# Kernel optimization log

Measured on AMD Instinct MI355X. Metric: run time of the kernel, lower is better.

The kernel has to match this reference:

```python
import jax, jax.numpy as jnp
import numpy as np


def _conv2d(x, w, b, pad, rhs_dilation=(1, 1)):
    out = jax.lax.conv_general_dilated(
        x, w, window_strides=(1, 1),
        padding=((pad, pad), (pad, pad)),
        rhs_dilation=rhs_dilation,
        dimension_numbers=('NCHW', 'OIHW', 'NCHW'))
    return out + b[None, :, None, None]


def _bilinear(img, gx, gy):
    # img [C,H,W]; gx,gy [9,h,w] in [-1,1]; grid_sample bilinear, align_corners=True.
    # Coords are pre-clamped to [-1,1] so all samples are in-bounds; clamped
    # neighbor indices get zero bilinear weight at the boundary, matching torch.
    C, H, W = img.shape
    ix = (gx + 1.0) * 0.5 * (W - 1)
    iy = (gy + 1.0) * 0.5 * (H - 1)
    x0 = jnp.floor(ix)
    y0 = jnp.floor(iy)
    wx = ix - x0
    wy = iy - y0
    x0i = jnp.clip(x0.astype(jnp.int32), 0, W - 1)
    x1i = jnp.clip(x0i + 1, 0, W - 1)
    y0i = jnp.clip(y0.astype(jnp.int32), 0, H - 1)
    y1i = jnp.clip(y0i + 1, 0, H - 1)
    v00 = img[:, y0i, x0i]
    v01 = img[:, y0i, x1i]
    v10 = img[:, y1i, x0i]
    v11 = img[:, y1i, x1i]
    return (v00 * (1 - wx) * (1 - wy) + v01 * wx * (1 - wy)
            + v10 * (1 - wx) * wy + v11 * wx * wy)  # [C,9,h,w]


def _forward(x, conv_w, conv_b, offset_w, offset_b, mod_w, mod_b):
    b, c, h, w = x.shape
    offset = _conv2d(x, offset_w, offset_b, pad=1)          # [b,18,h,w]
    gx = jnp.clip(offset[:, :9] + jnp.linspace(-1.0, 1.0, w)[None, None, None, :], -1.0, 1.0)
    gy = jnp.clip(offset[:, 9:] + jnp.linspace(-1.0, 1.0, h)[None, None, :, None], -1.0, 1.0)
    sampled = jax.vmap(_bilinear)(x, gx, gy)                # [b,c,9,h,w]
    mod = _conv2d(x, mod_w, mod_b, pad=1)                   # [b,9,h,w]
    interp = sampled * mod[:, None]                         # [b,c,9,h,w]
    # tile the 9 samples into a 3h x 3w spatial grid: sample k = i + j*3 goes to block (j, i)
    tiled = interp.reshape(b, c, 3, 3, h, w).transpose(0, 1, 2, 4, 3, 5).reshape(b, c, 3 * h, 3 * w)
    # dilated 3x3 conv with dilation (h+1, w+1), stride 1, padding 1 -> [b,oc,h,w]
    return _conv2d(tiled, conv_w, conv_b, pad=1, rhs_dilation=(h + 1, w + 1))


def setup_inputs() -> dict:
    key = jax.random.key(0)
    ks = jax.random.split(key, 7)
    B, C, OC, H, W = 8, 256, 256, 64, 64
    return {
        'x': jax.random.normal(ks[0], (B, C, H, W), jnp.float32),
        'conv_w': jax.random.normal(ks[1], (OC, C, 3, 3), jnp.float32) * 0.02,
        'conv_b': jax.random.normal(ks[2], (OC,), jnp.float32) * 0.02,
        'offset_w': jax.random.normal(ks[3], (18, C, 3, 3), jnp.float32) * 0.01,
        'offset_b': jax.random.normal(ks[4], (18,), jnp.float32) * 0.01,
        'mod_w': jax.random.normal(ks[5], (9, C, 3, 3), jnp.float32) * 0.02,
        'mod_b': jax.random.normal(ks[6], (9,), jnp.float32) * 0.02,
    }


def reference(x, conv_w, conv_b, offset_w, offset_b, mod_w, mod_b):
    return _forward(x, conv_w, conv_b, offset_w, offset_b, mod_w, mod_b)
```

## Files before the change

kernel.cpp:

```cpp
#include <hip/hip_runtime.h>

typedef __attribute__((ext_vector_type(8))) _Float16 f16x8;
typedef __attribute__((ext_vector_type(4))) float f32x4;

#define CB 8
#define CC 256
#define CHW 4096


__global__ __launch_bounds__(256) void prep_k(const float* __restrict__ convw,
                                              const float* __restrict__ offw,
                                              const float* __restrict__ modw,
                                              _Float16* __restrict__ wAf,
                                              _Float16* __restrict__ wAomF) {
    int i = blockIdx.x * 256 + threadIdx.x;
    {
        int lane = i & 63, tile = (i >> 6) & 15, cc = (i >> 10) & 7, t = i >> 13;
        int oc = tile * 16 + (lane & 15);
        int cb = cc * 32 + (lane >> 4) * 8;
        f16x8 v;
#pragma unroll
        for (int j = 0; j < 8; ++j)
            v[j] = (_Float16)convw[oc * 2304 + (cb + j) * 9 + t];
        *(f16x8*)(wAf + (size_t)i * 8) = v;
    }
    if (i < 9216) {
        int lane = i & 63, tile = (i >> 6) & 1, cc = (i >> 7) & 7, t = i >> 10;
        int mr = tile * 16 + (lane & 15);
        int cb = cc * 32 + (lane >> 4) * 8;
        f16x8 u;
#pragma unroll
        for (int j = 0; j < 8; ++j) {
            int c = cb + j;
            float vv = 0.f;
            if (mr < 18) vv = offw[(mr * 256 + c) * 9 + t];
            else if (mr < 27) vv = modw[((mr - 18) * 256 + c) * 9 + t];
            u[j] = (_Float16)vv;
        }
        *(f16x8*)(wAomF + (size_t)i * 8) = u;
    }
}

__global__ __launch_bounds__(256) void xk(const float* __restrict__ x,
                                          _Float16* __restrict__ xt) {
    __shared__ ushort tile[64][264];
    int bid = blockIdx.x;
    int b = bid & 7, pos0 = (bid >> 3) << 6;
    int tid = threadIdx.x;
    int p = tid & 63;
    const float* xb = x + ((size_t)b << 20);
#pragma unroll 4
    for (int rep = 0; rep < 64; rep++) {
        int c = rep * 4 + (tid >> 6);
        _Float16 h = (_Float16)xb[((size_t)c << 12) + pos0 + p];
        tile[p][c] = __builtin_bit_cast(ushort, h);
    }
    __syncthreads();
    _Float16* xtb = xt + ((size_t)b << 20);
#pragma unroll
    for (int rep = 0; rep < 8; rep++) {
        int item = rep * 256 + tid;
        int pp = item >> 5, ch = item & 31;
        f16x8 v = *(const f16x8*)((const char*)&tile[0][0] + pp * 528 + ch * 16);
        *(f16x8*)((char*)xtb + (((size_t)(pos0 + pp)) << 9) + ch * 16) = v;
    }
}

__global__ __launch_bounds__(256) void k1(const _Float16* __restrict__ xt,
                                          const _Float16* __restrict__ wAomF,
                                          const float* __restrict__ offb,
                                          const float* __restrict__ modb,
                                          float4* __restrict__ descW,
                                          int4* __restrict__ descO) {
    __shared__ float sEp[32][68];

    int bid = blockIdx.x;
    int b = bid & 7, y = bid >> 3;
    int tid = threadIdx.x;
    int lane = tid & 63;
    int w = __builtin_amdgcn_readfirstlane(tid >> 6);
    int l15 = lane & 15, oct = lane >> 4;

    const _Float16* xtb = xt + ((size_t)b << 20);
    int kylo = (y == 0) ? 1 : 0;
    int kyhi = (y == 63) ? 1 : 2;

    f32x4 acc[2];
    acc[0] = (f32x4)0.f;
    acc[1] = (f32x4)0.f;
    f16x8 Z = {};

    int px = (w << 4) + l15;

    for (int ty = kylo; ty <= kyhi; ++ty) {
        int yy = y + ty - 1;
#pragma unroll
        for (int tx = 0; tx < 3; ++tx) {
            int t = ty * 3 + tx;
            int xx = px + tx - 1;
            bool val = (xx >= 0 && xx < 64);
            int xxc = min(max(xx, 0), 63);
            const f16x8* bp = (const f16x8*)(xtb + (((yy << 6) + xxc) << 8) + oct * 8);
            const f16x8* wf = (const f16x8*)wAomF + (size_t)t * 16 * 64 + lane;
#pragma unroll
            for (int c0 = 0; c0 < 256; c0 += 32) {
                f16x8 bf = bp[c0 >> 3];
                if (!val) bf = Z;
                int cc = c0 >> 5;
#pragma unroll
                for (int m = 0; m < 2; m++) {
                    f16x8 af = wf[(cc * 2 + m) * 64];
                    acc[m] = __builtin_amdgcn_mfma_f32_16x16x32_f16(af, bf, acc[m], 0, 0, 0);
                }
            }
        }
    }

#pragma unroll
    for (int m = 0; m < 2; m++) {
#pragma unroll
        for (int r = 0; r < 4; r++) {
            int row = (m << 4) + (oct << 2) + r;
            if (row < 27) sEp[row][px] = acc[m][r];
        }
    }
    __syncthreads();

    int g = tid >> 6;
    int xx2 = tid & 63;
    if (g < 3) {
        float lx = -1.0f + xx2 * (2.0f / 63.0f);
        float ly = -1.0f + y * (2.0f / 63.0f);
#pragma unroll
        for (int j = 0; j < 3; j++) {
            int k = g * 3 + j;
            float gx = sEp[k][xx2] + offb[k] + lx;
            gx = fminf(fmaxf(gx, -1.f), 1.f);
            float gy = sEp[9 + k][xx2] + offb[9 + k] + ly;
            gy = fminf(fmaxf(gy, -1.f), 1.f);
            float m = sEp[18 + k][xx2] + modb[k];
            float ix = (gx + 1.0f) * 0.5f * 63.0f;
            float iy = (gy + 1.0f) * 0.5f * 63.0f;
            float fx = floorf(ix), fy = floorf(iy);
            float wx = ix - fx, wy = iy - fy;
            int x0 = min(max((int)fx, 0), 63);
            int x1 = min(x0 + 1, 63);
            int y0 = min(max((int)fy, 0), 63);
            int y1 = min(y0 + 1, 63);
            float w00 = (1.f - wx) * (1.f - wy) * m;
            float w01 = wx * (1.f - wy) * m;
            float w10 = (1.f - wx) * wy * m;
            float w11 = wx * wy * m;
            int di = ((b * 9 + k) << 12) + (y << 6) + xx2;
            descW[di] = make_float4(w00, w01, w10, w11);
            descO[di] = make_int4(((y0 << 6) + x0) << 9, ((y0 << 6) + x1) << 9,
                                  ((y1 << 6) + x0) << 9, ((y1 << 6) + x1) << 9);
        }
    }
}

struct SmK2 {
    char cmb[2][2][8192];
    float4 dW[2][64];
    int4 dO[2][64];
};
__global__ __launch_bounds__(512, 4) void k2(const _Float16* __restrict__ xt,
                                             const _Float16* __restrict__ wAf,
                                             const float4* __restrict__ descW,
                                             const int4* __restrict__ descO,
                                             const float* __restrict__ convb,
                                             float* __restrict__ out) {
    __shared__ union SU {
        SmK2 m;
        f32x4 sred[2048];
    } S;

    int bid = blockIdx.x;
    int b = bid & 7, oy = bid >> 3;
    int tid = threadIdx.x;
    int l = tid & 63;
    int wid = __builtin_amdgcn_readfirstlane(tid >> 6);
    int mgrp = wid & 3, ks = wid >> 2;
    int oct = l >> 4, l15 = l & 15;

    const char* xtb = (const char*)(xt + ((size_t)b << 20));

    f32x4 acc[4][4];
#pragma unroll
    for (int mt = 0; mt < 4; mt++)
#pragma unroll
        for (int nt = 0; nt < 4; nt++) acc[mt][nt] = (f32x4)0.f;

    int p_ox = (tid >> 3) & 63;
    int p_cs = tid & 7;
    int csl = (p_ox << 7) + ((p_cs ^ (p_ox & 7)) << 4);
    const char* xtb_cs = xtb + p_cs * 16;

    int boff = (l15 << 7) + ((((ks << 2) + oct) ^ (l15 & 7)) << 4);

    auto stage_desc = [&](int t) {
        int slot = t & 1;
        int xx = tid;
        int ky = t / 3, kx = t % 3;
        int yy = oy + ky - 1;
        int xp = xx + kx - 1;
        float4 w4s = make_float4(0.f, 0.f, 0.f, 0.f);
        int4 o4 = make_int4(0, 0, 0, 0);
        if (yy >= 0 && yy < 64 && xp >= 0 && xp < 64) {
            int di = ((b * 9 + t) << 12) + (yy << 6) + xp;
            w4s = descW[di];
            o4 = descO[di];
        }
        S.m.dW[slot][xx] = w4s;
        S.m.dO[slot][xx] = o4;
    };

    int rdo0, rdo1, rdo2, rdo3;
    _Float16 rh0, rh1, rh2, rh3;
    auto refresh_desc = [&](int t) {
        int slot = t & 1;
        int4 o4 = S.m.dO[slot][p_ox];
        rdo0 = o4.x; rdo1 = o4.y; rdo2 = o4.z; rdo3 = o4.w;
        float4 w4 = S.m.dW[slot][p_ox];
        rh0 = (_Float16)w4.x; rh1 = (_Float16)w4.y;
        rh2 = (_Float16)w4.z; rh3 = (_Float16)w4.w;
    };

    auto issue_q = [&](f16x8* cr, int q) {
        const char* base = xtb_cs + (q << 7);
        cr[0] = *(const f16x8*)(base + rdo0);
        cr[1] = *(const f16x8*)(base + rdo1);
        cr[2] = *(const f16x8*)(base + rdo2);
        cr[3] = *(const f16x8*)(base + rdo3);
    };

    auto comb_write = [&](const f16x8* cr, char* dst) {
        f16x8 W0 = {rh0, rh0, rh0, rh0, rh0, rh0, rh0, rh0};
        f16x8 W1 = {rh1, rh1, rh1, rh1, rh1, rh1, rh1, rh1};
        f16x8 W2 = {rh2, rh2, rh2, rh2, rh2, rh2, rh2, rh2};
        f16x8 W3 = {rh3, rh3, rh3, rh3, rh3, rh3, rh3, rh3};
        f16x8 r = cr[0] * W0 + cr[1] * W1 + cr[2] * W2 + cr[3] * W3;
        *(f16x8*)(dst + csl) = r;
    };

    auto load_afr = [&](f16x8* afr, int m) {
        int t = m >> 2, q = m & 3;
        const f16x8* wf = (const f16x8*)wAf +
                          ((size_t)((t * 8 + q * 2 + ks) * 16 + mgrp * 4)) * 64 + l;
        afr[0] = wf[0];
        afr[1] = wf[64];
        afr[2] = wf[128];
        afr[3] = wf[192];
    };

    auto do_mfma = [&](const char* src, const f16x8* afr) {
        f16x8 bfr[4];
#pragma unroll
        for (int nt = 0; nt < 4; ++nt)
            bfr[nt] = *(const f16x8*)(src + boff + (nt << 11));
#pragma unroll
        for (int nt = 0; nt < 4; ++nt)
#pragma unroll
            for (int mt = 0; mt < 4; ++mt)
                acc[mt][nt] = __builtin_amdgcn_mfma_f32_16x16x32_f16(
                    afr[mt], bfr[nt], acc[mt][nt], 0, 0, 0);
    };

    if (tid < 64) stage_desc(0);
    __syncthreads();
    refresh_desc(0);
    {
        f16x8 c0[4];
        issue_q(c0, 0);
        comb_write(c0, S.m.cmb[0][0]);
        issue_q(c0, 1);
        comb_write(c0, S.m.cmb[0][1]);
    }
    __syncthreads();

    for (int P = 0; P < 18; ++P) {
        int pb = P & 1;
        int t = P >> 1;
        bool more = (P < 17);

        if (!(P & 1)) {
            if (t + 1 <= 8 && tid < 64) stage_desc(t + 1);
        } else if (more) {
            refresh_desc((P + 1) >> 1);
        }

        f16x8 afr[4];
        f16x8 cr[4];

        load_afr(afr, 2 * P);
        if (more) issue_q(cr, (2 * P + 2) & 3);
        do_mfma(S.m.cmb[pb][0], afr);
        load_afr(afr, 2 * P + 1);
        if (more) comb_write(cr, S.m.cmb[pb ^ 1][0]);

        if (more) issue_q(cr, (2 * P + 3) & 3);
        do_mfma(S.m.cmb[pb][1], afr);
        if (more) comb_write(cr, S.m.cmb[pb ^ 1][1]);

        __syncthreads();
    }

#pragma unroll
    for (int R = 0; R < 2; ++R) {
        if (ks == 1) {
#pragma unroll
            for (int mtl = 0; mtl < 2; ++mtl) {
#pragma unroll
                for (int nt = 0; nt < 4; ++nt) {
                    int fi = (((mgrp << 1) + mtl) << 8) + (((nt << 4) + l15) << 2) + oct;
                    S.sred[fi] = acc[(R << 1) + mtl][nt];
                }
            }
        }
        __syncthreads();
        if (ks == 0) {
#pragma unroll
            for (int mtl = 0; mtl < 2; ++mtl) {
#pragma unroll
                for (int nt = 0; nt < 4; ++nt) {
                    int fi = (((mgrp << 1) + mtl) << 8) + (((nt << 4) + l15) << 2) + oct;
                    acc[(R << 1) + mtl][nt] += S.sred[fi];
                }
            }
        }
        __syncthreads();
    }

    if (ks == 0) {
        size_t outb = ((size_t)b << 20);
#pragma unroll
        for (int mt = 0; mt < 4; ++mt) {
#pragma unroll
            for (int nt = 0; nt < 4; ++nt) {
                int ox = (nt << 4) + l15;
#pragma unroll
                for (int r = 0; r < 4; ++r) {
                    int oc = (mgrp << 6) + (mt << 4) + (oct << 2) + r;
                    out[outb + (size_t)oc * 4096 + (oy << 6) + ox] = acc[mt][nt][r] + convb[oc];
                }
            }
        }
    }
}

extern "C" void kernel_launch(void* const* d_in, const int* in_sizes, int n_in,
                              void* d_out, int out_size, void* d_ws, size_t ws_size,
                              hipStream_t stream) {
    const float* x     = (const float*)d_in[0];
    const float* convw = (const float*)d_in[1];
    const float* convb = (const float*)d_in[2];
    const float* offw  = (const float*)d_in[3];
    const float* offb  = (const float*)d_in[4];
    const float* modw  = (const float*)d_in[5];
    const float* modb  = (const float*)d_in[6];
    float* out = (float*)d_out;

    char* ws = (char*)d_ws;
    _Float16* wAf   = (_Float16*)(ws);
    _Float16* wAomF = (_Float16*)(ws + 1179648);
    float4*   descW = (float4*)(ws + 1327104);
    int4*     descO = (int4*)(ws + 6045696);
    _Float16* xt    = (_Float16*)(ws + 10764288);

    hipLaunchKernelGGL(prep_k, dim3(288), dim3(256), 0, stream, convw, offw, modw, wAf, wAomF);
    hipLaunchKernelGGL(xk, dim3(512), dim3(256), 0, stream, x, xt);
    hipLaunchKernelGGL(k1, dim3(512), dim3(256), 0, stream, xt, wAomF, offb, modb, descW, descO);
    hipLaunchKernelGGL(k2, dim3(512), dim3(512), 0, stream, xt, wAf, descW, descO, convb, out);
}
```

Baseline: 103.1 us.

## Deepen k2 software pipeline with register-prefetched descriptors and double-buffered A fragments

Restructures the main loop of k2 so that gathers for the next half-stage are issued a full iteration ahead. A-fragment weights are double-buffered in registers (afrA/afrB), and descriptor global loads are split from their shared-memory stores so their latency is hidden across the MFMA work. Each phase now processes two 8KB combine chunks at once. This raises register pressure, so launch bounds drop from 4 to 2 blocks per CU, trading occupancy for more instruction-level overlap.

```diff
diff --git a/kernel.cpp b/kernel.cpp
--- a/kernel.cpp
+++ b/kernel.cpp
@@ -160,11 +160,11 @@
 }
 
 struct SmK2 {
-    char cmb[2][2][8192];
+    char cmb[2][16384];
     float4 dW[2][64];
     int4 dO[2][64];
 };
-__global__ __launch_bounds__(512, 4) void k2(const _Float16* __restrict__ xt,
+__global__ __launch_bounds__(512, 2) void k2(const _Float16* __restrict__ xt,
                                              const _Float16* __restrict__ wAf,
                                              const float4* __restrict__ descW,
                                              const int4* __restrict__ descO,
@@ -198,25 +198,29 @@
 
     int boff = (l15 << 7) + ((((ks << 2) + oct) ^ (l15 & 7)) << 4);
 
-    auto stage_desc = [&](int t) {
-        int slot = t & 1;
-        int xx = tid;
+    float4 sdw;
+    int4 sdo;
+    auto stage_load = [&](int t) {
         int ky = t / 3, kx = t % 3;
         int yy = oy + ky - 1;
-        int xp = xx + kx - 1;
-        float4 w4s = make_float4(0.f, 0.f, 0.f, 0.f);
-        int4 o4 = make_int4(0, 0, 0, 0);
+        int xp = tid + kx - 1;
+        sdw = make_float4(0.f, 0.f, 0.f, 0.f);
+        sdo = make_int4(0, 0, 0, 0);
         if (yy >= 0 && yy < 64 && xp >= 0 && xp < 64) {
             int di = ((b * 9 + t) << 12) + (yy << 6) + xp;
-            w4s = descW[di];
-            o4 = descO[di];
-        }
-        S.m.dW[slot][xx] = w4s;
-        S.m.dO[slot][xx] = o4;
+            sdw = descW[di];
+            sdo = descO[di];
+        }
+    };
+    auto stage_store = [&](int t) {
+        int slot = t & 1;
+        S.m.dW[slot][tid] = sdw;
+        S.m.dO[slot][tid] = sdo;
     };
 
     int rdo0, rdo1, rdo2, rdo3;
     _Float16 rh0, rh1, rh2, rh3;
+    _Float16 rc0, rc1, rc2, rc3;
     auto refresh_desc = [&](int t) {
         int slot = t & 1;
         int4 o4 = S.m.dO[slot][p_ox];
@@ -226,83 +230,102 @@
         rh2 = (_Float16)w4.z; rh3 = (_Float16)w4.w;
     };
 
-    auto issue_q = [&](f16x8* cr, int q) {
-        const char* base = xtb_cs + (q << 7);
-        cr[0] = *(const f16x8*)(base + rdo0);
-        cr[1] = *(const f16x8*)(base + rdo1);
-        cr[2] = *(const f16x8*)(base + rdo2);
-        cr[3] = *(const f16x8*)(base + rdo3);
-    };
-
-    auto comb_write = [&](const f16x8* cr, char* dst) {
-        f16x8 W0 = {rh0, rh0, rh0, rh0, rh0, rh0, rh0, rh0};
-        f16x8 W1 = {rh1, rh1, rh1, rh1, rh1, rh1, rh1, rh1};
-        f16x8 W2 = {rh2, rh2, rh2, rh2, rh2, rh2, rh2, rh2};
-        f16x8 W3 = {rh3, rh3, rh3, rh3, rh3, rh3, rh3, rh3};
-        f16x8 r = cr[0] * W0 + cr[1] * W1 + cr[2] * W2 + cr[3] * W3;
-        *(f16x8*)(dst + csl) = r;
-    };
-
-    auto load_afr = [&](f16x8* afr, int m) {
-        int t = m >> 2, q = m & 3;
-        const f16x8* wf = (const f16x8*)wAf +
-                          ((size_t)((t * 8 + q * 2 + ks) * 16 + mgrp * 4)) * 64 + l;
-        afr[0] = wf[0];
-        afr[1] = wf[64];
-        afr[2] = wf[128];
-        afr[3] = wf[192];
-    };
-
-    auto do_mfma = [&](const char* src, const f16x8* afr) {
-        f16x8 bfr[4];
-#pragma unroll
-        for (int nt = 0; nt < 4; ++nt)
-            bfr[nt] = *(const f16x8*)(src + boff + (nt << 11));
-#pragma unroll
-        for (int nt = 0; nt < 4; ++nt)
-#pragma unroll
-            for (int mt = 0; mt < 4; ++mt)
-                acc[mt][nt] = __builtin_amdgcn_mfma_f32_16x16x32_f16(
-                    afr[mt], bfr[nt], acc[mt][nt], 0, 0, 0);
-    };
-
-    if (tid < 64) stage_desc(0);
+    f16x8 cr[4][2];
+    auto issue_G = [&](int h) {
+        const char* base = xtb_cs + (h << 8);
+#pragma unroll
+        for (int j = 0; j < 2; ++j) {
+            cr[0][j] = *(const f16x8*)(base + rdo0 + j * 128);
+            cr[1][j] = *(const f16x8*)(base + rdo1 + j * 128);
+            cr[2][j] = *(const f16x8*)(base + rdo2 + j * 128);
+            cr[3][j] = *(const f16x8*)(base + rdo3 + j * 128);
+        }
+        rc0 = rh0; rc1 = rh1; rc2 = rh2; rc3 = rh3;
+    };
+
+    auto combine = [&](char* dst) {
+        f16x8 W0 = {rc0, rc0, rc0, rc0, rc0, rc0, rc0, rc0};
+        f16x8 W1 = {rc1, rc1, rc1, rc1, rc1, rc1, rc1, rc1};
+        f16x8 W2 = {rc2, rc2, rc2, rc2, rc2, rc2, rc2, rc2};
+        f16x8 W3 = {rc3, rc3, rc3, rc3, rc3, rc3, rc3, rc3};
+#pragma unroll
+        for (int j = 0; j < 2; ++j) {
+            f16x8 r = cr[0][j] * W0 + cr[1][j] * W1 + cr[2][j] * W2 + cr[3][j] * W3;
+            *(f16x8*)(dst + (j << 13) + csl) = r;
+        }
+    };
+
+    auto load_afr = [&](f16x8 (&afr)[2][4], int Pn) {
+        int t = Pn >> 1, h = Pn & 1;
+#pragma unroll
+        for (int j = 0; j < 2; ++j) {
+            int q = 2 * h + j;
+            const f16x8* wf = (const f16x8*)wAf +
+                              ((size_t)((t * 8 + q * 2 + ks) * 16 + mgrp * 4)) * 64 + l;
+            afr[j][0] = wf[0];
+            afr[j][1] = wf[64];
+            afr[j][2] = wf[128];
+            afr[j][3] = wf[192];
+        }
+    };
+
+    auto do_mfma = [&](const char* src, f16x8 (&afr)[2][4]) {
+#pragma unroll
+        for (int j = 0; j < 2; ++j) {
+            f16x8 bfr[4];
+#pragma unroll
+            for (int nt = 0; nt < 4; ++nt)
+                bfr[nt] = *(const f16x8*)(src + (j << 13) + boff + (nt << 11));
+#pragma unroll
+            for (int nt = 0; nt < 4; ++nt)
+#pragma unroll
+                for (int mt = 0; mt < 4; ++mt)
+                    acc[mt][nt] = __builtin_amdgcn_mfma_f32_16x16x32_f16(
+                        afr[j][mt], bfr[nt], acc[mt][nt], 0, 0, 0);
+        }
+    };
+
+    f16x8 afrA[2][4], afrB[2][4];
+
+    if (tid < 64) {
+        stage_load(0);
+        stage_store(0);
+        stage_load(1);
+        stage_store(1);
+    }
     __syncthreads();
     refresh_desc(0);
-    {
-        f16x8 c0[4];
-        issue_q(c0, 0);
-        comb_write(c0, S.m.cmb[0][0]);
-        issue_q(c0, 1);
-        comb_write(c0, S.m.cmb[0][1]);
-    }
+    issue_G(0);
+    load_afr(afrA, 0);
+    combine(S.m.cmb[0]);
+    issue_G(1);
     __syncthreads();
 
-    for (int P = 0; P < 18; ++P) {
+    auto body = [&](int P, f16x8 (&cur)[2][4], f16x8 (&nxt)[2][4]) {
         int pb = P & 1;
-        int t = P >> 1;
-        bool more = (P < 17);
-
-        if (!(P & 1)) {
-            if (t + 1 <= 8 && tid < 64) stage_desc(t + 1);
-        } else if (more) {
-            refresh_desc((P + 1) >> 1);
-        }
-
-        f16x8 afr[4];
-        f16x8 cr[4];
-
-        load_afr(afr, 2 * P);
-        if (more) issue_q(cr, (2 * P + 2) & 3);
-        do_mfma(S.m.cmb[pb][0], afr);
-        load_afr(afr, 2 * P + 1);
-        if (more) comb_write(cr, S.m.cmb[pb ^ 1][0]);
-
-        if (more) issue_q(cr, (2 * P + 3) & 3);
-        do_mfma(S.m.cmb[pb][1], afr);
-        if (more) comb_write(cr, S.m.cmb[pb ^ 1][1]);
+        bool odd = (P & 1) != 0;
+
+        if (odd && P <= 13 && tid < 64) stage_load((P + 3) >> 1);
+
+        if (P < 17) combine(S.m.cmb[pb ^ 1]);
+
+        if (P < 16 && !odd) refresh_desc((P >> 1) + 1);
+
+        if (P < 16) issue_G(pb);
+
+        if (P < 17) load_afr(nxt, P + 1);
+
+        do_mfma(S.m.cmb[pb], cur);
+
+        if (odd && P <= 13 && tid < 64) stage_store((P + 3) >> 1);
 
         __syncthreads();
+    };
+
+#pragma unroll 1
+    for (int PP = 0; PP < 9; ++PP) {
+        body(2 * PP, afrA, afrB);
+        body(2 * PP + 1, afrB, afrA);
     }
 
 #pragma unroll
```

Measured after the change: 108.2 us. 1.05x slower.

## Merge weight-prep and transpose kernels, split work into finer blocks

Applied to the files above, without the earlier changes.

Merges the weight-conversion kernel and the x-transpose kernel into one launch, so one kernel launch and one inter-kernel gap go away. The transpose now handles half the channels per block, which doubles its block count and shrinks its shared tile. k1 is split into half-row blocks of 128 threads, giving twice as many blocks with smaller LDS. The main k2 loop also gets unroll 2, which risks raising register pressure.

```diff
diff --git a/kernel.cpp b/kernel.cpp
--- a/kernel.cpp
+++ b/kernel.cpp
@@ -8,74 +8,81 @@
 #define CHW 4096
 
 
-__global__ __launch_bounds__(256) void prep_k(const float* __restrict__ convw,
-                                              const float* __restrict__ offw,
-                                              const float* __restrict__ modw,
-                                              _Float16* __restrict__ wAf,
-                                              _Float16* __restrict__ wAomF) {
-    int i = blockIdx.x * 256 + threadIdx.x;
-    {
-        int lane = i & 63, tile = (i >> 6) & 15, cc = (i >> 10) & 7, t = i >> 13;
-        int oc = tile * 16 + (lane & 15);
-        int cb = cc * 32 + (lane >> 4) * 8;
-        f16x8 v;
-#pragma unroll
-        for (int j = 0; j < 8; ++j)
-            v[j] = (_Float16)convw[oc * 2304 + (cb + j) * 9 + t];
-        *(f16x8*)(wAf + (size_t)i * 8) = v;
-    }
-    if (i < 9216) {
-        int lane = i & 63, tile = (i >> 6) & 1, cc = (i >> 7) & 7, t = i >> 10;
-        int mr = tile * 16 + (lane & 15);
-        int cb = cc * 32 + (lane >> 4) * 8;
-        f16x8 u;
-#pragma unroll
-        for (int j = 0; j < 8; ++j) {
-            int c = cb + j;
-            float vv = 0.f;
-            if (mr < 18) vv = offw[(mr * 256 + c) * 9 + t];
-            else if (mr < 27) vv = modw[((mr - 18) * 256 + c) * 9 + t];
-            u[j] = (_Float16)vv;
-        }
-        *(f16x8*)(wAomF + (size_t)i * 8) = u;
-    }
-}
-
-__global__ __launch_bounds__(256) void xk(const float* __restrict__ x,
-                                          _Float16* __restrict__ xt) {
-    __shared__ ushort tile[64][264];
+__global__ __launch_bounds__(256) void pxk(const float* __restrict__ x,
+                                           const float* __restrict__ convw,
+                                           const float* __restrict__ offw,
+                                           const float* __restrict__ modw,
+                                           _Float16* __restrict__ wAf,
+                                           _Float16* __restrict__ wAomF,
+                                           _Float16* __restrict__ xt) {
+    __shared__ ushort tile[64][136];
     int bid = blockIdx.x;
-    int b = bid & 7, pos0 = (bid >> 3) << 6;
     int tid = threadIdx.x;
+
+    if (bid < 288) {
+        int i = bid * 256 + tid;
+        {
+            int lane = i & 63, tl = (i >> 6) & 15, cc = (i >> 10) & 7, t = i >> 13;
+            int oc = tl * 16 + (lane & 15);
+            int cb = cc * 32 + (lane >> 4) * 8;
+            f16x8 v;
+#pragma unroll
+            for (int j = 0; j < 8; ++j)
+                v[j] = (_Float16)convw[oc * 2304 + (cb + j) * 9 + t];
+            *(f16x8*)(wAf + (size_t)i * 8) = v;
+        }
+        if (i < 9216) {
+            int lane = i & 63, tl = (i >> 6) & 1, cc = (i >> 7) & 7, t = i >> 10;
+            int mr = tl * 16 + (lane & 15);
+            int cb = cc * 32 + (lane >> 4) * 8;
+            f16x8 u;
+#pragma unroll
+            for (int j = 0; j < 8; ++j) {
+                int c = cb + j;
+                float vv = 0.f;
+                if (mr < 18) vv = offw[(mr * 256 + c) * 9 + t];
+                else if (mr < 27) vv = modw[((mr - 18) * 256 + c) * 9 + t];
+                u[j] = (_Float16)vv;
+            }
+            *(f16x8*)(wAomF + (size_t)i * 8) = u;
+        }
+        return;
+    }
+
+    int nb = bid - 288;
+    int b = nb & 7, g = nb >> 3;
+    int pos0 = (g >> 1) << 6;
+    int ch0 = (g & 1) << 7;
     int p = tid & 63;
     const float* xb = x + ((size_t)b << 20);
 #pragma unroll 4
-    for (int rep = 0; rep < 64; rep++) {
-        int c = rep * 4 + (tid >> 6);
+    for (int rep = 0; rep < 32; rep++) {
+        int c = ch0 + rep * 4 + (tid >> 6);
         _Float16 h = (_Float16)xb[((size_t)c << 12) + pos0 + p];
-        tile[p][c] = __builtin_bit_cast(ushort, h);
+        tile[p][c - ch0] = __builtin_bit_cast(ushort, h);
     }
     __syncthreads();
     _Float16* xtb = xt + ((size_t)b << 20);
 #pragma unroll
-    for (int rep = 0; rep < 8; rep++) {
+    for (int rep = 0; rep < 4; rep++) {
         int item = rep * 256 + tid;
-        int pp = item >> 5, ch = item & 31;
-        f16x8 v = *(const f16x8*)((const char*)&tile[0][0] + pp * 528 + ch * 16);
-        *(f16x8*)((char*)xtb + (((size_t)(pos0 + pp)) << 9) + ch * 16) = v;
+        int pp = item >> 4, c16 = item & 15;
+        f16x8 v = *(const f16x8*)((const char*)&tile[0][0] + pp * 272 + c16 * 16);
+        *(f16x8*)((char*)xtb + (((size_t)(pos0 + pp)) << 9) + (ch0 << 1) + (c16 << 4)) = v;
     }
 }
 
-__global__ __launch_bounds__(256) void k1(const _Float16* __restrict__ xt,
+__global__ __launch_bounds__(128) void k1(const _Float16* __restrict__ xt,
                                           const _Float16* __restrict__ wAomF,
                                           const float* __restrict__ offb,
                                           const float* __restrict__ modb,
                                           float4* __restrict__ descW,
                                           int4* __restrict__ descO) {
-    __shared__ float sEp[32][68];
+    __shared__ float sEp[32][36];
 
     int bid = blockIdx.x;
-    int b = bid & 7, y = bid >> 3;
+    int b = bid & 7, yx = bid >> 3;
+    int y = yx >> 1, xh = yx & 1;
     int tid = threadIdx.x;
     int lane = tid & 63;
     int w = __builtin_amdgcn_readfirstlane(tid >> 6);
@@ -90,7 +97,8 @@
     acc[1] = (f32x4)0.f;
     f16x8 Z = {};
 
-    int px = (w << 4) + l15;
+    int pxl = (w << 4) + l15;
+    int px = (xh << 5) + pxl;
 
     for (int ty = kylo; ty <= kyhi; ++ty) {
         int yy = y + ty - 1;
@@ -121,24 +129,25 @@
 #pragma unroll
         for (int r = 0; r < 4; r++) {
             int row = (m << 4) + (oct << 2) + r;
-            if (row < 27) sEp[row][px] = acc[m][r];
+            if (row < 27) sEp[row][pxl] = acc[m][r];
         }
     }
     __syncthreads();
 
-    int g = tid >> 6;
-    int xx2 = tid & 63;
-    if (g < 3) {
+    int gq = tid >> 5;
+    int xl = tid & 31;
+    if (gq < 3) {
+        int xx2 = (xh << 5) + xl;
         float lx = -1.0f + xx2 * (2.0f / 63.0f);
         float ly = -1.0f + y * (2.0f / 63.0f);
 #pragma unroll
         for (int j = 0; j < 3; j++) {
-            int k = g * 3 + j;
-            float gx = sEp[k][xx2] + offb[k] + lx;
+            int k = gq * 3 + j;
+            float gx = sEp[k][xl] + offb[k] + lx;
             gx = fminf(fmaxf(gx, -1.f), 1.f);
-            float gy = sEp[9 + k][xx2] + offb[9 + k] + ly;
+            float gy = sEp[9 + k][xl] + offb[9 + k] + ly;
             gy = fminf(fmaxf(gy, -1.f), 1.f);
-            float m = sEp[18 + k][xx2] + modb[k];
+            float m = sEp[18 + k][xl] + modb[k];
             float ix = (gx + 1.0f) * 0.5f * 63.0f;
             float iy = (gy + 1.0f) * 0.5f * 63.0f;
             float fx = floorf(ix), fy = floorf(iy);
@@ -278,6 +287,7 @@
     }
     __syncthreads();
 
+#pragma unroll 2
     for (int P = 0; P < 18; ++P) {
         int pb = P & 1;
         int t = P >> 1;
@@ -367,8 +377,7 @@
     int4*     descO = (int4*)(ws + 6045696);
     _Float16* xt    = (_Float16*)(ws + 10764288);
 
-    hipLaunchKernelGGL(prep_k, dim3(288), dim3(256), 0, stream, convw, offw, modw, wAf, wAomF);
-    hipLaunchKernelGGL(xk, dim3(512), dim3(256), 0, stream, x, xt);
-    hipLaunchKernelGGL(k1, dim3(512), dim3(256), 0, stream, xt, wAomF, offb, modb, descW, descO);
+    hipLaunchKernelGGL(pxk, dim3(1312), dim3(256), 0, stream, x, convw, offw, modw, wAf, wAomF, xt);
+    hipLaunchKernelGGL(k1, dim3(1024), dim3(128), 0, stream, xt, wAomF, offb, modb, descW, descO);
     hipLaunchKernelGGL(k2, dim3(512), dim3(512), 0, stream, xt, wAf, descW, descO, convb, out);
 }
```

Measured after the change: 164.6 us. +59.7%, slower.
